# Kernel optimization log

Hardware: AMD Instinct MI355X
Metric: run time of the kernel (lower is better)

## Reference

```python
import jax, jax.numpy as jnp
import numpy as np


def setup_inputs() -> dict:
    key = jax.random.key(0)
    ks = jax.random.split(key, 7)
    B, U, I, D, K = 16384, 100000, 1000000, 64, 16
    F = 2 * D
    stdv = 1.0 / np.sqrt(D)
    return {
        "user": jax.random.randint(ks[0], (B,), 0, U),
        "item": jax.random.randint(ks[1], (B,), 0, I),
        "user_emb": jax.random.normal(ks[2], (U, D), jnp.float32) * stdv,
        "item_emb": jax.random.normal(ks[3], (I, D), jnp.float32) * stdv,
        "w1": jax.random.normal(ks[4], (F, 1), jnp.float32) * stdv,
        "b1": jax.random.normal(ks[5], (1,), jnp.float32) * stdv,
        "v": jax.random.normal(ks[6], (F, K), jnp.float32) * stdv,
    }


def reference(user, item, user_emb, item_emb, w1, b1, v):
    # x: [B, 2*dim]
    x = jnp.concatenate([user_emb[user], item_emb[item]], axis=-1)
    # first-order term: Linear(feat_dim, 1) then squeeze -> [B]
    lin = (x @ w1 + b1)[:, 0]
    # second-order: sum_{i<j} x_i x_j (v v^T)_{ij}
    # == 0.5 * sum_k ((x @ v)_k^2 - (x^2 @ v^2)_k)  (FM identity)
    xv = x @ v                      # [B, k]
    x2v2 = (x * x) @ (v * v)        # [B, k]
    pair = 0.5 * jnp.sum(xv * xv - x2v2, axis=-1)
    return lin + pair
```

## Files before the change

kernel.cpp:

```cpp
#include <hip/hip_runtime.h>

#define DIMS 64
#define KF 16
#define F 128

template<int CTRL>
__device__ __forceinline__ float dppmv(float x) {
    return __builtin_bit_cast(float,
        __builtin_amdgcn_update_dpp(0, __builtin_bit_cast(int, x), CTRL, 0xF, 0xF, true));
}
template<int PAT>
__device__ __forceinline__ float swzf(float x) {
    return __builtin_bit_cast(float,
        __builtin_amdgcn_ds_swizzle(__builtin_bit_cast(int, x), PAT));
}

#define DPP_XOR1  0xB1
#define DPP_XOR2  0x4E
#define DPP_XOR8  0x128
#define SWZ_XOR4  0x101F
#define SWZ_XOR16 0x401F

__device__ __forceinline__ float sum_xor16(float x) {
#if __has_builtin(__builtin_amdgcn_permlane16_swap)
    auto r = __builtin_amdgcn_permlane16_swap(__builtin_bit_cast(int, x),
                                              __builtin_bit_cast(int, x), false, false);
    return __builtin_bit_cast(float, (int)r[0]) + __builtin_bit_cast(float, (int)r[1]);
#else
    return x + swzf<SWZ_XOR16>(x);
#endif
}
__device__ __forceinline__ float sum_xor32(float x) {
#if __has_builtin(__builtin_amdgcn_permlane32_swap)
    auto r = __builtin_amdgcn_permlane32_swap(__builtin_bit_cast(int, x),
                                              __builtin_bit_cast(int, x), false, false);
    return __builtin_bit_cast(float, (int)r[0]) + __builtin_bit_cast(float, (int)r[1]);
#else
    return x + __shfl_xor(x, 32, 64);
#endif
}

__global__ __launch_bounds__(256, 8) void fm_fwd_kernel(
    const int* __restrict__ user,
    const int* __restrict__ item,
    const float* __restrict__ user_emb,
    const float* __restrict__ item_emb,
    const float* __restrict__ w1,
    const float* __restrict__ b1,
    const float* __restrict__ v,
    float* __restrict__ out,
    int B)
{
    __shared__ float vsT[KF * F];

    const int tid  = threadIdx.x;
    const int lane = tid & 63;
    const int wv   = tid >> 6;
    const int base = __builtin_amdgcn_readfirstlane((int)blockIdx.x * 8 + wv * 2);

    const int i0 = min(base,     B - 1);
    const int i1 = min(base + 1, B - 1);
    const int u0 = user[i0], t0 = item[i0];
    const int u1 = user[i1], t1 = item[i1];

    const float xa0 = user_emb[(size_t)u0 * DIMS + lane];
    const float xb0 = item_emb[(size_t)t0 * DIMS + lane];
    const float xa1 = user_emb[(size_t)u1 * DIMS + lane];
    const float xb1 = item_emb[(size_t)t1 * DIMS + lane];
    const float wa = w1[lane], wb = w1[DIMS + lane];
    const float bias = b1[0];

    {
        const float4* vg = (const float4*)v;
        float4 p0 = vg[tid * 2 + 0];
        float4 p1 = vg[tid * 2 + 1];
        const int f  = tid >> 1;
        const int k0 = (tid & 1) * 8;
        vsT[(k0+0)*F + f] = p0.x;  vsT[(k0+1)*F + f] = p0.y;
        vsT[(k0+2)*F + f] = p0.z;  vsT[(k0+3)*F + f] = p0.w;
        vsT[(k0+4)*F + f] = p1.x;  vsT[(k0+5)*F + f] = p1.y;
        vsT[(k0+6)*F + f] = p1.z;  vsT[(k0+7)*F + f] = p1.w;
    }
    asm volatile("s_waitcnt lgkmcnt(0)" ::: "memory");
    __builtin_amdgcn_s_barrier();

    float s0[KF], s1[KF];
    float A = 0.f, Bq = 0.f;
    #pragma unroll
    for (int k = 0; k < KF; ++k) {
        const float va = vsT[k * F + lane];
        const float vb = vsT[k * F + DIMS + lane];
        A  += va * va;
        Bq += vb * vb;
        s0[k] = xa0 * va + xb0 * vb;
        s1[k] = xa1 * va + xb1 * vb;
    }
    float c0 = xa0*wa + xb0*wb - 0.5f*(xa0*xa0*A + xb0*xb0*Bq);
    float c1 = xa1*wa + xb1*wb - 0.5f*(xa1*xa1*A + xb1*xb1*Bq);

    #define HALVE2(MV, M, N) { \
        const bool hi = (lane & (M)) != 0; \
        _Pragma("unroll") \
        for (int i = 0; i < (N); ++i) { \
            float k0_ = hi ? s0[(N)+i] : s0[i]; float d0_ = hi ? s0[i] : s0[(N)+i]; \
            float k1_ = hi ? s1[(N)+i] : s1[i]; float d1_ = hi ? s1[i] : s1[(N)+i]; \
            s0[i] = k0_ + MV(d0_); \
            s1[i] = k1_ + MV(d1_); \
        } }
    HALVE2(dppmv<DPP_XOR1>, 1, 8)
    HALVE2(dppmv<DPP_XOR2>, 2, 4)
    HALVE2(dppmv<DPP_XOR8>, 8, 2)
    HALVE2(swzf<SWZ_XOR4>,  4, 1)
    #undef HALVE2

    float sv0 = sum_xor32(sum_xor16(s0[0]));
    float sv1 = sum_xor32(sum_xor16(s1[0]));

    c0 += 0.125f * sv0 * sv0;
    c1 += 0.125f * sv1 * sv1;

    c0 += dppmv<DPP_XOR1>(c0);  c1 += dppmv<DPP_XOR1>(c1);
    c0 += dppmv<DPP_XOR2>(c0);  c1 += dppmv<DPP_XOR2>(c1);
    c0 += swzf<SWZ_XOR4>(c0);   c1 += swzf<SWZ_XOR4>(c1);
    c0 += dppmv<DPP_XOR8>(c0);  c1 += dppmv<DPP_XOR8>(c1);
    c0 = sum_xor16(c0);         c1 = sum_xor16(c1);
    c0 = sum_xor32(c0);         c1 = sum_xor32(c1);

    if (lane == 0) {
        if (base + 1 < B) {
            *(float2*)&out[base] = make_float2(bias + c0, bias + c1);
        } else if (base < B) {
            out[base] = bias + c0;
        }
    }
}

extern "C" void kernel_launch(void* const* d_in, const int* in_sizes, int n_in,
                              void* d_out, int out_size, void* d_ws, size_t ws_size,
                              hipStream_t stream) {
    const int*   user     = (const int*)  d_in[0];
    const int*   item     = (const int*)  d_in[1];
    const float* user_emb = (const float*)d_in[2];
    const float* item_emb = (const float*)d_in[3];
    const float* w1       = (const float*)d_in[4];
    const float* b1       = (const float*)d_in[5];
    const float* v        = (const float*)d_in[6];
    float* out = (float*)d_out;

    const int B = in_sizes[0];
    const int blocks = (B + 7) / 8;
    fm_fwd_kernel<<<blocks, 256, 0, stream>>>(user, item, user_emb, item_emb,
                                              w1, b1, v, out, B);
}
```

Baseline: 10.40 us.

## Process four rows per wavefront and merge final reductions across rows

```diff
diff --git a/kernel.cpp b/kernel.cpp
--- a/kernel.cpp
+++ b/kernel.cpp
@@ -3,6 +3,7 @@
 #define DIMS 64
 #define KF 16
 #define F 128
+#define ROWS 4
 
 template<int CTRL>
 __device__ __forceinline__ float dppmv(float x) {
@@ -40,7 +41,7 @@
 #endif
 }
 
-__global__ __launch_bounds__(256, 8) void fm_fwd_kernel(
+__global__ __launch_bounds__(256, 4) void fm_fwd_kernel(
     const int* __restrict__ user,
     const int* __restrict__ item,
     const float* __restrict__ user_emb,
@@ -56,17 +57,22 @@
     const int tid  = threadIdx.x;
     const int lane = tid & 63;
     const int wv   = tid >> 6;
-    const int base = __builtin_amdgcn_readfirstlane((int)blockIdx.x * 8 + wv * 2);
+    const int base = __builtin_amdgcn_readfirstlane((int)blockIdx.x * (4*ROWS) + wv * ROWS);
 
-    const int i0 = min(base,     B - 1);
-    const int i1 = min(base + 1, B - 1);
-    const int u0 = user[i0], t0 = item[i0];
-    const int u1 = user[i1], t1 = item[i1];
+    int ui[ROWS], ti[ROWS];
+    #pragma unroll
+    for (int r = 0; r < ROWS; ++r) {
+        const int i = min(base + r, B - 1);
+        ui[r] = user[i];
+        ti[r] = item[i];
+    }
 
-    const float xa0 = user_emb[(size_t)u0 * DIMS + lane];
-    const float xb0 = item_emb[(size_t)t0 * DIMS + lane];
-    const float xa1 = user_emb[(size_t)u1 * DIMS + lane];
-    const float xb1 = item_emb[(size_t)t1 * DIMS + lane];
+    float xa[ROWS], xb[ROWS];
+    #pragma unroll
+    for (int r = 0; r < ROWS; ++r) {
+        xa[r] = user_emb[(size_t)ui[r] * DIMS + lane];
+        xb[r] = item_emb[(size_t)ti[r] * DIMS + lane];
+    }
     const float wa = w1[lane], wb = w1[DIMS + lane];
     const float bias = b1[0];
 
@@ -84,7 +90,7 @@
     asm volatile("s_waitcnt lgkmcnt(0)" ::: "memory");
     __builtin_amdgcn_s_barrier();
 
-    float s0[KF], s1[KF];
+    float s0[KF], s1[KF], s2[KF], s3[KF];
     float A = 0.f, Bq = 0.f;
     #pragma unroll
     for (int k = 0; k < KF; ++k) {
@@ -92,46 +98,63 @@
         const float vb = vsT[k * F + DIMS + lane];
         A  += va * va;
         Bq += vb * vb;
-        s0[k] = xa0 * va + xb0 * vb;
-        s1[k] = xa1 * va + xb1 * vb;
+        s0[k] = xa[0] * va + xb[0] * vb;
+        s1[k] = xa[1] * va + xb[1] * vb;
+        s2[k] = xa[2] * va + xb[2] * vb;
+        s3[k] = xa[3] * va + xb[3] * vb;
     }
-    float c0 = xa0*wa + xb0*wb - 0.5f*(xa0*xa0*A + xb0*xb0*Bq);
-    float c1 = xa1*wa + xb1*wb - 0.5f*(xa1*xa1*A + xb1*xb1*Bq);
+    float c[ROWS];
+    #pragma unroll
+    for (int r = 0; r < ROWS; ++r)
+        c[r] = xa[r]*wa + xb[r]*wb - 0.5f*(xa[r]*xa[r]*A + xb[r]*xb[r]*Bq);
 
-    #define HALVE2(MV, M, N) { \
+    #define HALVE2(SA, SB, MV, M, N) { \
         const bool hi = (lane & (M)) != 0; \
         _Pragma("unroll") \
         for (int i = 0; i < (N); ++i) { \
-            float k0_ = hi ? s0[(N)+i] : s0[i]; float d0_ = hi ? s0[i] : s0[(N)+i]; \
-            float k1_ = hi ? s1[(N)+i] : s1[i]; float d1_ = hi ? s1[i] : s1[(N)+i]; \
-            s0[i] = k0_ + MV(d0_); \
-            s1[i] = k1_ + MV(d1_); \
+            float kA = hi ? SA[(N)+i] : SA[i]; float dA = hi ? SA[i] : SA[(N)+i]; \
+            float kB = hi ? SB[(N)+i] : SB[i]; float dB = hi ? SB[i] : SB[(N)+i]; \
+            SA[i] = kA + MV(dA); \
+            SB[i] = kB + MV(dB); \
         } }
-    HALVE2(dppmv<DPP_XOR1>, 1, 8)
-    HALVE2(dppmv<DPP_XOR2>, 2, 4)
-    HALVE2(dppmv<DPP_XOR8>, 8, 2)
-    HALVE2(swzf<SWZ_XOR4>,  4, 1)
+    #define REDUCE_PAIR(SA, SB, CA, CB) { \
+        HALVE2(SA, SB, dppmv<DPP_XOR1>, 1, 8) \
+        HALVE2(SA, SB, dppmv<DPP_XOR2>, 2, 4) \
+        HALVE2(SA, SB, dppmv<DPP_XOR8>, 8, 2) \
+        HALVE2(SA, SB, swzf<SWZ_XOR4>,  4, 1) \
+        float svA = sum_xor32(sum_xor16(SA[0])); \
+        float svB = sum_xor32(sum_xor16(SB[0])); \
+        CA += 0.125f * svA * svA; \
+        CB += 0.125f * svB * svB; \
+    }
+    REDUCE_PAIR(s0, s1, c[0], c[1])
+    REDUCE_PAIR(s2, s3, c[2], c[3])
+    #undef REDUCE_PAIR
     #undef HALVE2
 
-    float sv0 = sum_xor32(sum_xor16(s0[0]));
-    float sv1 = sum_xor32(sum_xor16(s1[0]));
+    float r0, r1;
+    {
+        const bool hi = (lane & 1) != 0;
+        float k0 = hi ? c[2] : c[0], d0 = hi ? c[0] : c[2];
+        float k1 = hi ? c[3] : c[1], d1 = hi ? c[1] : c[3];
+        r0 = k0 + dppmv<DPP_XOR1>(d0);
+        r1 = k1 + dppmv<DPP_XOR1>(d1);
+    }
+    float rr;
+    {
+        const bool hi = (lane & 2) != 0;
+        float kk = hi ? r1 : r0, dd = hi ? r0 : r1;
+        rr = kk + dppmv<DPP_XOR2>(dd);
+    }
+    rr += swzf<SWZ_XOR4>(rr);
+    rr += dppmv<DPP_XOR8>(rr);
+    rr = sum_xor16(rr);
+    rr = sum_xor32(rr);
 
-    c0 += 0.125f * sv0 * sv0;
-    c1 += 0.125f * sv1 * sv1;
-
-    c0 += dppmv<DPP_XOR1>(c0);  c1 += dppmv<DPP_XOR1>(c1);
-    c0 += dppmv<DPP_XOR2>(c0);  c1 += dppmv<DPP_XOR2>(c1);
-    c0 += swzf<SWZ_XOR4>(c0);   c1 += swzf<SWZ_XOR4>(c1);
-    c0 += dppmv<DPP_XOR8>(c0);  c1 += dppmv<DPP_XOR8>(c1);
-    c0 = sum_xor16(c0);         c1 = sum_xor16(c1);
-    c0 = sum_xor32(c0);         c1 = sum_xor32(c1);
-
-    if (lane == 0) {
-        if (base + 1 < B) {
-            *(float2*)&out[base] = make_float2(bias + c0, bias + c1);
-        } else if (base < B) {
-            out[base] = bias + c0;
-        }
+    if (lane < ROWS) {
+        const int row = ((lane & 1) << 1) | ((lane >> 1) & 1);
+        if (base + row < B)
+            out[base + row] = bias + rr;
     }
 }
 
@@ -148,7 +171,8 @@
     float* out = (float*)d_out;
 
     const int B = in_sizes[0];
-    const int blocks = (B + 7) / 8;
+    const int rows_per_block = 4 * ROWS;
+    const int blocks = (B + rows_per_block - 1) / rows_per_block;
     fm_fwd_kernel<<<blocks, 256, 0, stream>>>(user, item, user_emb, item_emb,
                                               w1, b1, v, out, B);
 }
```

New measurement: 9.735 us. 6.4% less time.
